# Optimization experiments

Measured on AMD Instinct MI355X. Metric: run time of the kernel, lower is better.

Reference implementation:

```python
import jax, jax.numpy as jnp
import numpy as np

N_NODES = 100000
N_EDGES = 1600000
D_FEAT = 48


def sage_conv(x, src, dst, Wl, Wr, b):
    # mean aggregation of neighbor messages x[src] at dst (PyG source_to_target)
    msg_sum = jax.ops.segment_sum(x[src], dst, num_segments=N_NODES)  # [N, d]
    cnt = jax.ops.segment_sum(jnp.ones((src.shape[0],), x.dtype), dst,
                              num_segments=N_NODES)  # [N]
    mean = msg_sum / jnp.maximum(cnt, 1.0)[:, None]
    # out = lin_l(mean neighbors) + lin_r(self); bias only on lin_l (PyG default)
    return mean @ Wl + b + x @ Wr


def setup_inputs() -> dict:
    key = jax.random.key(0)
    ks = jax.random.split(key, 8)
    x = jax.random.normal(ks[0], (N_NODES, D_FEAT), jnp.float32)
    edge_index = jax.random.randint(ks[1], (2, N_EDGES), 0, N_NODES, jnp.int64)
    def w(k, fi, fo):
        return jax.random.normal(k, (fi, fo), jnp.float32) / np.sqrt(fi)
    return {
        "x": x,
        "edge_index": edge_index,
        "W1l": w(ks[2], D_FEAT, 32), "W1r": w(ks[3], D_FEAT, 32),
        "b1": jnp.zeros((32,), jnp.float32),
        "W2l": w(ks[4], 32, 16), "W2r": w(ks[5], 32, 16),
        "b2": jnp.zeros((16,), jnp.float32),
        "Wlin": w(ks[6], 16, 2), "blin": jnp.zeros((2,), jnp.float32),
    }


def reference(x, edge_index, W1l, W1r, b1, W2l, W2r, b2, Wlin, blin):
    src, dst = edge_index[0], edge_index[1]
    h = jax.nn.relu(sage_conv(x, src, dst, W1l, W1r, b1))
    h = jax.nn.relu(sage_conv(h, src, dst, W2l, W2r, b2))
    return h @ Wlin + blin  # [N, 2] logits
```

## Files before the change

### kernel.cpp

```cpp
#include <hip/hip_runtime.h>
#include <hip/hip_bf16.h>


constexpr int NN  = 100000;
constexpr int NE  = 1600000;
constexpr int NCH = (NN + 255) / 256;
constexpr int NB  = 391;
constexpr int CAP = 4608;
constexpr int SEG = CAP + 3 * 256;
constexpr int T1  = 2048;
constexpr int EPT = T1 / 256;
constexpr int NB1 = (NE + T1 - 1) / T1;

__device__ __forceinline__ float bl(unsigned u) { return __uint_as_float(u << 16); }
__device__ __forceinline__ float bh(unsigned u) { return __uint_as_float(u & 0xffff0000u); }
__device__ __forceinline__ unsigned f2b(float x) {
    unsigned u = __float_as_uint(x);
    return (u + 0x7fffu + ((u >> 16) & 1u)) >> 16;
}
__device__ __forceinline__ unsigned pack2(float a, float b) {
    return f2b(a) | (f2b(b) << 16);
}

__device__ __forceinline__ int wave_incl_scan(int v, int lane) {
#pragma unroll
    for (int d = 1; d < 64; d <<= 1) {
        int t = __shfl_up(v, d, 64);
        if (lane >= d) v += t;
    }
    return v;
}

__global__ __launch_bounds__(256) void k1_kernel(
    const float* __restrict__ X,
    const float* __restrict__ Wl,
    const float* __restrict__ Wr,
    const int*   __restrict__ ei,
    int* __restrict__ bsize, unsigned* __restrict__ bbuf,
    __hip_bfloat16* __restrict__ P, __hip_bfloat16* __restrict__ R)
{
    __shared__ float sW[2][48 * 32];
    __shared__ int hist[NB], base[NB], cur[NB];
    __shared__ int s_any;

    if (blockIdx.x < NCH) {
        for (int i = threadIdx.x; i < 48 * 32; i += 256) {
            sW[0][i] = Wl[i];
            sW[1][i] = Wr[i];
        }
        __syncthreads();
        int n = blockIdx.x * 256 + threadIdx.x;
        if (n > NN) return;
        if (n == NN) {
            uint4 z = make_uint4(0, 0, 0, 0);
            uint4* pp = reinterpret_cast<uint4*>(P + (size_t)NN * 32);
#pragma unroll
            for (int i = 0; i < 4; ++i) pp[i] = z;
            return;
        }
        float xr[48];
        const float4* xp = reinterpret_cast<const float4*>(X + (size_t)n * 48);
#pragma unroll
        for (int i = 0; i < 12; ++i) {
            float4 u = xp[i];
            xr[i*4+0] = u.x; xr[i*4+1] = u.y; xr[i*4+2] = u.z; xr[i*4+3] = u.w;
        }
        float accp[32], accr[32];
#pragma unroll
        for (int j = 0; j < 32; ++j) { accp[j] = 0.f; accr[j] = 0.f; }
#pragma unroll
        for (int k = 0; k < 48; ++k) {
            float xk = xr[k];
#pragma unroll
            for (int j = 0; j < 32; ++j) {
                accp[j] += xk * sW[0][k * 32 + j];
                accr[j] += xk * sW[1][k * 32 + j];
            }
        }
        uint4* pp = reinterpret_cast<uint4*>(P + (size_t)n * 32);
        uint4* rp = reinterpret_cast<uint4*>(R + (size_t)n * 32);
#pragma unroll
        for (int i = 0; i < 4; ++i) {
            uint4 u, v;
            u.x = pack2(accp[i*8+0], accp[i*8+1]); u.y = pack2(accp[i*8+2], accp[i*8+3]);
            u.z = pack2(accp[i*8+4], accp[i*8+5]); u.w = pack2(accp[i*8+6], accp[i*8+7]);
            v.x = pack2(accr[i*8+0], accr[i*8+1]); v.y = pack2(accr[i*8+2], accr[i*8+3]);
            v.z = pack2(accr[i*8+4], accr[i*8+5]); v.w = pack2(accr[i*8+6], accr[i*8+7]);
            pp[i] = u;
            rp[i] = v;
        }
    } else {
        if (threadIdx.x == 0) s_any = 0;
        for (int i = threadIdx.x; i < NB; i += 256) { hist[i] = 0; cur[i] = 0; }
        __syncthreads();
        int dv = 0;
        for (int i = threadIdx.x; i < 2048; i += 256) dv |= ei[2 * i + 1];
        if (dv != 0) atomicOr(&s_any, 1);
        __syncthreads();
        int sh = (s_any == 0) ? 1 : 0;

        int e0 = (blockIdx.x - NCH) * T1;
        int sreg[EPT], dreg[EPT];
#pragma unroll
        for (int it = 0; it < EPT; ++it) {
            int e = e0 + it * 256 + threadIdx.x;
            bool ok = e < NE;
            int s = ok ? ei[(size_t)e << sh] : -1;
            int d = ok ? ei[(size_t)(NE + e) << sh] : -1;
            if ((unsigned)s >= (unsigned)NN || (unsigned)d >= (unsigned)NN) { s = -1; d = -1; }
            sreg[it] = s; dreg[it] = d;
            if (d >= 0) atomicAdd(&hist[d >> 8], 1);
        }
        __syncthreads();
        for (int b = threadIdx.x; b < NB; b += 256) {
            int h = hist[b];
            base[b] = h ? atomicAdd(&bsize[b], h) : 0;
        }
        __syncthreads();
#pragma unroll
        for (int it = 0; it < EPT; ++it) {
            int s = sreg[it], d = dreg[it];
            if (d < 0) continue;
            int b = d >> 8;
            int pos = base[b] + atomicAdd(&cur[b], 1);
            if (pos < CAP)
                bbuf[(size_t)b * CAP + pos] = ((unsigned)s << 8) | (unsigned)(d & 255);
        }
    }
}

__global__ __launch_bounds__(256) void k2_kernel(
    const int* __restrict__ bsize, const unsigned* __restrict__ bbuf,
    int* __restrict__ deg, int* __restrict__ rowstart, int* __restrict__ csr_src)
{
    __shared__ int ldeg[256], lcur[256], ws[4];
    int b = blockIdx.x, t = threadIdx.x;
    int bs = b * SEG;

    int S = min(bsize[b], CAP);
    const unsigned* bp = bbuf + (size_t)b * CAP;
    ldeg[t] = 0;
    __syncthreads();
    for (int i = t; i < S; i += 256)
        atomicAdd(&ldeg[bp[i] & 255u], 1);
    __syncthreads();

    int v  = ldeg[t];
    int pv = (v + 3) & ~3;
    int lane = t & 63, wid = t >> 6;
    int incl = wave_incl_scan(pv, lane);
    if (lane == 63) ws[wid] = incl;
    __syncthreads();
    int off = 0;
#pragma unroll
    for (int w = 0; w < 3; ++w)
        if (wid > w) off += ws[w];
    int excl = off + incl - pv;

    int node = (b << 8) + t;
    if (node < NN) {
        deg[node] = v;
        rowstart[node] = bs + excl;
    }
    lcur[t] = excl;
    __syncthreads();

    for (int i = t; i < S; i += 256) {
        unsigned pk = bp[i];
        int pos = atomicAdd(&lcur[pk & 255u], 1);
        csr_src[bs + pos] = (int)(pk >> 8);
    }
    for (int p = excl + v; p < excl + pv; ++p)
        csr_src[bs + p] = NN;
}

__global__ __launch_bounds__(256) void gather1f_kernel(
    const int* __restrict__ rowstart, const int* __restrict__ deg,
    const int* __restrict__ csr_src,
    const __hip_bfloat16* __restrict__ p1,
    const __hip_bfloat16* __restrict__ r1,
    const float* __restrict__ b1,
    const float* __restrict__ W2l,
    const float* __restrict__ W2r,
    __hip_bfloat16* __restrict__ P2,
    __hip_bfloat16* __restrict__ R2)
{
    __shared__ float sW2l[32 * 16], sW2r[32 * 16], sb1[32];
    __shared__ float shh[32 * 64];
    int t = threadIdx.x;
    for (int i = t; i < 32 * 16; i += 256) { sW2l[i] = W2l[i]; sW2r[i] = W2r[i]; }
    if (t < 32) sb1[t] = b1[t];
    __syncthreads();

    int loc = t >> 2, c = t & 3;
    int n = blockIdx.x * 64 + loc;
    bool valid = n < NN;

    if (valid) {
        int start = rowstart[n], dn = deg[n];
        int pv4 = ((dn + 3) & ~3) >> 2;
        float acc[8];
#pragma unroll
        for (int j = 0; j < 8; ++j) acc[j] = 0.f;
        const uint4* prow = reinterpret_cast<const uint4*>(p1);
        const int4* cp4 = reinterpret_cast<const int4*>(csr_src + start);
        for (int k = 0; k < pv4; ++k) {
            int4 s4 = cp4[k];
            uint4 a = prow[(size_t)s4.x * 4 + c];
            uint4 b = prow[(size_t)s4.y * 4 + c];
            uint4 d = prow[(size_t)s4.z * 4 + c];
            uint4 e = prow[(size_t)s4.w * 4 + c];
            acc[0] += bl(a.x) + bl(b.x) + bl(d.x) + bl(e.x);
            acc[1] += bh(a.x) + bh(b.x) + bh(d.x) + bh(e.x);
            acc[2] += bl(a.y) + bl(b.y) + bl(d.y) + bl(e.y);
            acc[3] += bh(a.y) + bh(b.y) + bh(d.y) + bh(e.y);
            acc[4] += bl(a.z) + bl(b.z) + bl(d.z) + bl(e.z);
            acc[5] += bh(a.z) + bh(b.z) + bh(d.z) + bh(e.z);
            acc[6] += bl(a.w) + bl(b.w) + bl(d.w) + bl(e.w);
            acc[7] += bh(a.w) + bh(b.w) + bh(d.w) + bh(e.w);
        }
        float inv = 1.0f / fmaxf((float)dn, 1.0f);
        uint4 r = reinterpret_cast<const uint4*>(r1)[(size_t)n * 4 + c];
        float rr[8] = { bl(r.x), bh(r.x), bl(r.y), bh(r.y),
                        bl(r.z), bh(r.z), bl(r.w), bh(r.w) };
#pragma unroll
        for (int j = 0; j < 8; ++j)
            shh[(c * 8 + j) * 64 + loc] = fmaxf(acc[j] * inv + rr[j] + sb1[c * 8 + j], 0.f);
    }
    __syncthreads();

    if (valid) {
        float accp[4], accr[4];
#pragma unroll
        for (int j = 0; j < 4; ++j) { accp[j] = 0.f; accr[j] = 0.f; }
#pragma unroll
        for (int k = 0; k < 32; ++k) {
            float hk = shh[k * 64 + loc];
#pragma unroll
            for (int j = 0; j < 4; ++j) {
                accp[j] += hk * sW2l[k * 16 + c * 4 + j];
                accr[j] += hk * sW2r[k * 16 + c * 4 + j];
            }
        }
        uint2 up, ur;
        up.x = pack2(accp[0], accp[1]); up.y = pack2(accp[2], accp[3]);
        ur.x = pack2(accr[0], accr[1]); ur.y = pack2(accr[2], accr[3]);
        reinterpret_cast<uint2*>(P2)[(size_t)n * 4 + c] = up;
        reinterpret_cast<uint2*>(R2)[(size_t)n * 4 + c] = ur;
    } else if (n == NN) {
        uint2 z = make_uint2(0, 0);
        reinterpret_cast<uint2*>(P2)[(size_t)NN * 4 + c] = z;
        reinterpret_cast<uint2*>(R2)[(size_t)NN * 4 + c] = z;
    }
}

__global__ __launch_bounds__(256) void gather2_kernel(
    const int* __restrict__ rowstart, const int* __restrict__ deg,
    const int* __restrict__ csr_src,
    const __hip_bfloat16* __restrict__ P2,
    const __hip_bfloat16* __restrict__ R2,
    const float* __restrict__ b2,
    const float* __restrict__ Wlin,
    const float* __restrict__ blin,
    float* __restrict__ out)
{
    __shared__ float sb[16], sW[32], sbl[2];
    if (threadIdx.x < 16) sb[threadIdx.x] = b2[threadIdx.x];
    else if (threadIdx.x < 48) sW[threadIdx.x - 16] = Wlin[threadIdx.x - 16];
    else if (threadIdx.x < 50) sbl[threadIdx.x - 48] = blin[threadIdx.x - 48];
    __syncthreads();
    int t = blockIdx.x * 256 + threadIdx.x;
    int n = t >> 1, c = t & 1;
    if (n >= NN) return;
    int start = rowstart[n], dn = deg[n];
    int pv4 = ((dn + 3) & ~3) >> 2;

    float acc[8];
#pragma unroll
    for (int j = 0; j < 8; ++j) acc[j] = 0.f;
    const uint4* prow = reinterpret_cast<const uint4*>(P2);
    const int4* cp4 = reinterpret_cast<const int4*>(csr_src + start);
    for (int k = 0; k < pv4; ++k) {
        int4 s4 = cp4[k];
        uint4 a = prow[(size_t)s4.x * 2 + c];
        uint4 b = prow[(size_t)s4.y * 2 + c];
        uint4 d = prow[(size_t)s4.z * 2 + c];
        uint4 e = prow[(size_t)s4.w * 2 + c];
        acc[0] += bl(a.x) + bl(b.x) + bl(d.x) + bl(e.x);
        acc[1] += bh(a.x) + bh(b.x) + bh(d.x) + bh(e.x);
        acc[2] += bl(a.y) + bl(b.y) + bl(d.y) + bl(e.y);
        acc[3] += bh(a.y) + bh(b.y) + bh(d.y) + bh(e.y);
        acc[4] += bl(a.z) + bl(b.z) + bl(d.z) + bl(e.z);
        acc[5] += bh(a.z) + bh(b.z) + bh(d.z) + bh(e.z);
        acc[6] += bl(a.w) + bl(b.w) + bl(d.w) + bl(e.w);
        acc[7] += bh(a.w) + bh(b.w) + bh(d.w) + bh(e.w);
    }
    float inv = 1.0f / fmaxf((float)dn, 1.0f);
    uint4 r = reinterpret_cast<const uint4*>(R2)[(size_t)n * 2 + c];
    float rr[8] = { bl(r.x), bh(r.x), bl(r.y), bh(r.y),
                    bl(r.z), bh(r.z), bl(r.w), bh(r.w) };
    float o0 = 0.f, o1 = 0.f;
#pragma unroll
    for (int j = 0; j < 8; ++j) {
        int kk = c * 8 + j;
        float hv = fmaxf(acc[j] * inv + rr[j] + sb[kk], 0.f);
        o0 += hv * sW[kk * 2];
        o1 += hv * sW[kk * 2 + 1];
    }
    o0 += __shfl_xor(o0, 1, 64);
    o1 += __shfl_xor(o1, 1, 64);
    if (c == 0)
        reinterpret_cast<float2*>(out)[n] = make_float2(o0 + sbl[0], o1 + sbl[1]);
}

extern "C" void kernel_launch(void* const* d_in, const int* in_sizes, int n_in,
                              void* d_out, int out_size, void* d_ws, size_t ws_size,
                              hipStream_t stream)
{
    const float* x    = (const float*)d_in[0];
    const int*   ei   = (const int*)d_in[1];
    const float* W1l  = (const float*)d_in[2];
    const float* W1r  = (const float*)d_in[3];
    const float* b1   = (const float*)d_in[4];
    const float* W2l  = (const float*)d_in[5];
    const float* W2r  = (const float*)d_in[6];
    const float* b2   = (const float*)d_in[7];
    const float* Wlin = (const float*)d_in[8];
    const float* blin = (const float*)d_in[9];
    float* out = (float*)d_out;

    char* wsb = (char*)d_ws;
    int*      bsize    = (int*)(wsb + 64);
    int*      deg      = (int*)(wsb + 4096);
    int*      rowstart = (int*)(wsb + 404096);
    int*      csr_src  = (int*)(wsb + 804096);
    unsigned* bbuf     = (unsigned*)(wsb + 9300000);
    __hip_bfloat16* p1 = (__hip_bfloat16*)(wsb + 16600000);
    __hip_bfloat16* r1 = (__hip_bfloat16*)(wsb + 23100000);
    __hip_bfloat16* p2 = (__hip_bfloat16*)(wsb + 29600000);
    __hip_bfloat16* r2 = (__hip_bfloat16*)(wsb + 32900000);

    dim3 blk(256);

    hipMemsetAsync(bsize, 0, NB * sizeof(int), stream);
    k1_kernel<<<NCH + NB1, blk, 0, stream>>>(x, W1l, W1r, ei, bsize, bbuf, p1, r1);
    k2_kernel<<<NB, blk, 0, stream>>>(bsize, bbuf, deg, rowstart, csr_src);
    gather1f_kernel<<<(NN + 1 + 63) / 64, blk, 0, stream>>>(
        rowstart, deg, csr_src, p1, r1, b1, W2l, W2r, p2, r2);
    gather2_kernel<<<(NN * 2 + 255) / 256, blk, 0, stream>>>(
        rowstart, deg, csr_src, p2, r2, b2, Wlin, blin, out);
}
```

Before: 187.1 us.

## Vectorize edge reads, split dense pass, widen CSR build, prefetch gather indices

```diff
diff --git a/kernel.cpp b/kernel.cpp
--- a/kernel.cpp
+++ b/kernel.cpp
@@ -9,7 +9,6 @@
 constexpr int CAP = 4608;
 constexpr int SEG = CAP + 3 * 256;
 constexpr int T1  = 2048;
-constexpr int EPT = T1 / 256;
 constexpr int NB1 = (NE + T1 - 1) / T1;
 
 __device__ __forceinline__ float bl(unsigned u) { return __uint_as_float(u << 16); }
@@ -31,7 +30,7 @@
     return v;
 }
 
-__global__ __launch_bounds__(256) void k1_kernel(
+__global__ __launch_bounds__(256, 6) void k1_kernel(
     const float* __restrict__ X,
     const float* __restrict__ Wl,
     const float* __restrict__ Wr,
@@ -40,7 +39,7 @@
     __hip_bfloat16* __restrict__ P, __hip_bfloat16* __restrict__ R)
 {
     __shared__ float sW[2][48 * 32];
-    __shared__ int hist[NB], base[NB], cur[NB];
+    __shared__ int hist[NB], base[NB];
     __shared__ int s_any;
 
     if (blockIdx.x < NCH) {
@@ -58,78 +57,108 @@
             for (int i = 0; i < 4; ++i) pp[i] = z;
             return;
         }
-        float xr[48];
         const float4* xp = reinterpret_cast<const float4*>(X + (size_t)n * 48);
-#pragma unroll
-        for (int i = 0; i < 12; ++i) {
-            float4 u = xp[i];
-            xr[i*4+0] = u.x; xr[i*4+1] = u.y; xr[i*4+2] = u.z; xr[i*4+3] = u.w;
-        }
-        float accp[32], accr[32];
-#pragma unroll
-        for (int j = 0; j < 32; ++j) { accp[j] = 0.f; accr[j] = 0.f; }
-#pragma unroll
-        for (int k = 0; k < 48; ++k) {
-            float xk = xr[k];
-#pragma unroll
-            for (int j = 0; j < 32; ++j) {
-                accp[j] += xk * sW[0][k * 32 + j];
-                accr[j] += xk * sW[1][k * 32 + j];
-            }
-        }
-        uint4* pp = reinterpret_cast<uint4*>(P + (size_t)n * 32);
-        uint4* rp = reinterpret_cast<uint4*>(R + (size_t)n * 32);
-#pragma unroll
-        for (int i = 0; i < 4; ++i) {
-            uint4 u, v;
-            u.x = pack2(accp[i*8+0], accp[i*8+1]); u.y = pack2(accp[i*8+2], accp[i*8+3]);
-            u.z = pack2(accp[i*8+4], accp[i*8+5]); u.w = pack2(accp[i*8+6], accp[i*8+7]);
-            v.x = pack2(accr[i*8+0], accr[i*8+1]); v.y = pack2(accr[i*8+2], accr[i*8+3]);
-            v.z = pack2(accr[i*8+4], accr[i*8+5]); v.w = pack2(accr[i*8+6], accr[i*8+7]);
-            pp[i] = u;
-            rp[i] = v;
+        float acc[32];
+#pragma unroll 1
+        for (int pass = 0; pass < 2; ++pass) {
+#pragma unroll
+            for (int j = 0; j < 32; ++j) acc[j] = 0.f;
+#pragma unroll
+            for (int i = 0; i < 12; ++i) {
+                float4 u = xp[i];
+                const float* w = &sW[pass][i * 4 * 32];
+#pragma unroll
+                for (int j = 0; j < 32; ++j) {
+                    acc[j] += u.x * w[j];
+                    acc[j] += u.y * w[32 + j];
+                    acc[j] += u.z * w[64 + j];
+                    acc[j] += u.w * w[96 + j];
+                }
+            }
+            __hip_bfloat16* dstp = pass ? R : P;
+            uint4* op = reinterpret_cast<uint4*>(dstp + (size_t)n * 32);
+#pragma unroll
+            for (int i = 0; i < 4; ++i) {
+                uint4 o;
+                o.x = pack2(acc[i*8+0], acc[i*8+1]);
+                o.y = pack2(acc[i*8+2], acc[i*8+3]);
+                o.z = pack2(acc[i*8+4], acc[i*8+5]);
+                o.w = pack2(acc[i*8+6], acc[i*8+7]);
+                op[i] = o;
+            }
         }
     } else {
         if (threadIdx.x == 0) s_any = 0;
-        for (int i = threadIdx.x; i < NB; i += 256) { hist[i] = 0; cur[i] = 0; }
+        for (int i = threadIdx.x; i < NB; i += 256) hist[i] = 0;
         __syncthreads();
         int dv = 0;
         for (int i = threadIdx.x; i < 2048; i += 256) dv |= ei[2 * i + 1];
         if (dv != 0) atomicOr(&s_any, 1);
         __syncthreads();
-        int sh = (s_any == 0) ? 1 : 0;
-
-        int e0 = (blockIdx.x - NCH) * T1;
-        int sreg[EPT], dreg[EPT];
-#pragma unroll
-        for (int it = 0; it < EPT; ++it) {
-            int e = e0 + it * 256 + threadIdx.x;
-            bool ok = e < NE;
-            int s = ok ? ei[(size_t)e << sh] : -1;
-            int d = ok ? ei[(size_t)(NE + e) << sh] : -1;
-            if ((unsigned)s >= (unsigned)NN || (unsigned)d >= (unsigned)NN) { s = -1; d = -1; }
-            sreg[it] = s; dreg[it] = d;
-            if (d >= 0) atomicAdd(&hist[d >> 8], 1);
-        }
+        const bool i64 = (s_any == 0);
+        const int e0 = (blockIdx.x - NCH) * T1;
+
+        auto sweep = [&](auto&& f) {
+            if (i64) {
+                const int4* sp = reinterpret_cast<const int4*>(ei) + (e0 >> 1);
+                const int4* dp = reinterpret_cast<const int4*>(ei) + ((NE + e0) >> 1);
+#pragma unroll
+                for (int it = 0; it < 4; ++it) {
+                    int p = it * 256 + threadIdx.x;
+                    int e = e0 + 2 * p;
+                    if (e + 2 <= NE) {
+                        int4 s4 = sp[p], d4 = dp[p];
+                        f(s4.x, d4.x);
+                        f(s4.z, d4.z);
+                    } else {
+                        for (int e2 = e; e2 < NE && e2 < e + 2; ++e2)
+                            f(ei[(size_t)e2 << 1], ei[(size_t)(NE + e2) << 1]);
+                    }
+                }
+            } else {
+                const int4* sp = reinterpret_cast<const int4*>(ei) + (e0 >> 2);
+                const int4* dp = reinterpret_cast<const int4*>(ei) + ((NE + e0) >> 2);
+#pragma unroll
+                for (int it = 0; it < 2; ++it) {
+                    int q = it * 256 + threadIdx.x;
+                    int e = e0 + 4 * q;
+                    if (e + 4 <= NE) {
+                        int4 s4 = sp[q], d4 = dp[q];
+                        f(s4.x, d4.x);
+                        f(s4.y, d4.y);
+                        f(s4.z, d4.z);
+                        f(s4.w, d4.w);
+                    } else {
+                        for (int e2 = e; e2 < NE && e2 < e + 4; ++e2)
+                            f(ei[e2], ei[NE + e2]);
+                    }
+                }
+            }
+        };
+
+        sweep([&](int s, int d) {
+            if ((unsigned)s < (unsigned)NN && (unsigned)d < (unsigned)NN)
+                atomicAdd(&hist[d >> 8], 1);
+        });
         __syncthreads();
         for (int b = threadIdx.x; b < NB; b += 256) {
             int h = hist[b];
             base[b] = h ? atomicAdd(&bsize[b], h) : 0;
         }
         __syncthreads();
-#pragma unroll
-        for (int it = 0; it < EPT; ++it) {
-            int s = sreg[it], d = dreg[it];
-            if (d < 0) continue;
-            int b = d >> 8;
-            int pos = base[b] + atomicAdd(&cur[b], 1);
-            if (pos < CAP)
-                bbuf[(size_t)b * CAP + pos] = ((unsigned)s << 8) | (unsigned)(d & 255);
-        }
-    }
-}
-
-__global__ __launch_bounds__(256) void k2_kernel(
+        sweep([&](int s, int d) {
+            if ((unsigned)s < (unsigned)NN && (unsigned)d < (unsigned)NN) {
+                int bk = d >> 8;
+                int pos = atomicAdd(&base[bk], 1);
+                if (pos < CAP)
+                    bbuf[(size_t)bk * CAP + pos] =
+                        ((unsigned)s << 8) | (unsigned)(d & 255);
+            }
+        });
+    }
+}
+
+__global__ __launch_bounds__(1024) void k2_kernel(
     const int* __restrict__ bsize, const unsigned* __restrict__ bbuf,
     int* __restrict__ deg, int* __restrict__ rowstart, int* __restrict__ csr_src)
 {
@@ -139,39 +168,43 @@
 
     int S = min(bsize[b], CAP);
     const unsigned* bp = bbuf + (size_t)b * CAP;
-    ldeg[t] = 0;
-    __syncthreads();
-    for (int i = t; i < S; i += 256)
+    if (t < 256) ldeg[t] = 0;
+    __syncthreads();
+    for (int i = t; i < S; i += 1024)
         atomicAdd(&ldeg[bp[i] & 255u], 1);
     __syncthreads();
 
-    int v  = ldeg[t];
-    int pv = (v + 3) & ~3;
-    int lane = t & 63, wid = t >> 6;
-    int incl = wave_incl_scan(pv, lane);
-    if (lane == 63) ws[wid] = incl;
-    __syncthreads();
-    int off = 0;
-#pragma unroll
-    for (int w = 0; w < 3; ++w)
-        if (wid > w) off += ws[w];
-    int excl = off + incl - pv;
-
-    int node = (b << 8) + t;
-    if (node < NN) {
-        deg[node] = v;
-        rowstart[node] = bs + excl;
-    }
-    lcur[t] = excl;
-    __syncthreads();
-
-    for (int i = t; i < S; i += 256) {
+    int v = 0, pv = 0, incl = 0, excl = 0;
+    if (t < 256) {
+        v  = ldeg[t];
+        pv = (v + 3) & ~3;
+        incl = wave_incl_scan(pv, t & 63);
+        if ((t & 63) == 63) ws[t >> 6] = incl;
+    }
+    __syncthreads();
+    if (t < 256) {
+        int off = 0, wid = t >> 6;
+#pragma unroll
+        for (int w = 0; w < 3; ++w)
+            if (wid > w) off += ws[w];
+        excl = off + incl - pv;
+        int node = (b << 8) + t;
+        if (node < NN) {
+            deg[node] = v;
+            rowstart[node] = bs + excl;
+        }
+        lcur[t] = excl;
+    }
+    __syncthreads();
+
+    for (int i = t; i < S; i += 1024) {
         unsigned pk = bp[i];
         int pos = atomicAdd(&lcur[pk & 255u], 1);
         csr_src[bs + pos] = (int)(pk >> 8);
     }
-    for (int p = excl + v; p < excl + pv; ++p)
-        csr_src[bs + p] = NN;
+    if (t < 256)
+        for (int p = excl + v; p < excl + pv; ++p)
+            csr_src[bs + p] = NN;
 }
 
 __global__ __launch_bounds__(256) void gather1f_kernel(
@@ -186,7 +219,7 @@
     __hip_bfloat16* __restrict__ R2)
 {
     __shared__ float sW2l[32 * 16], sW2r[32 * 16], sb1[32];
-    __shared__ float shh[32 * 64];
+    __shared__ float shh[32 * 65];
     int t = threadIdx.x;
     for (int i = t; i < 32 * 16; i += 256) { sW2l[i] = W2l[i]; sW2r[i] = W2r[i]; }
     if (t < 32) sb1[t] = b1[t];
@@ -199,13 +232,15 @@
     if (valid) {
         int start = rowstart[n], dn = deg[n];
         int pv4 = ((dn + 3) & ~3) >> 2;
-        float acc[8];
-#pragma unroll
-        for (int j = 0; j < 8; ++j) acc[j] = 0.f;
         const uint4* prow = reinterpret_cast<const uint4*>(p1);
         const int4* cp4 = reinterpret_cast<const int4*>(csr_src + start);
+        uint4 r = reinterpret_cast<const uint4*>(r1)[(size_t)n * 4 + c];
+        float acc[8];
+#pragma unroll
+        for (int j = 0; j < 8; ++j) acc[j] = 0.f;
+        int4 s4 = cp4[0];
         for (int k = 0; k < pv4; ++k) {
-            int4 s4 = cp4[k];
+            int4 nx = cp4[k + 1];
             uint4 a = prow[(size_t)s4.x * 4 + c];
             uint4 b = prow[(size_t)s4.y * 4 + c];
             uint4 d = prow[(size_t)s4.z * 4 + c];
@@ -218,14 +253,14 @@
             acc[5] += bh(a.z) + bh(b.z) + bh(d.z) + bh(e.z);
             acc[6] += bl(a.w) + bl(b.w) + bl(d.w) + bl(e.w);
             acc[7] += bh(a.w) + bh(b.w) + bh(d.w) + bh(e.w);
+            s4 = nx;
         }
         float inv = 1.0f / fmaxf((float)dn, 1.0f);
-        uint4 r = reinterpret_cast<const uint4*>(r1)[(size_t)n * 4 + c];
         float rr[8] = { bl(r.x), bh(r.x), bl(r.y), bh(r.y),
                         bl(r.z), bh(r.z), bl(r.w), bh(r.w) };
 #pragma unroll
         for (int j = 0; j < 8; ++j)
-            shh[(c * 8 + j) * 64 + loc] = fmaxf(acc[j] * inv + rr[j] + sb1[c * 8 + j], 0.f);
+            shh[(c * 8 + j) * 65 + loc] = fmaxf(acc[j] * inv + rr[j] + sb1[c * 8 + j], 0.f);
     }
     __syncthreads();
 
@@ -235,7 +270,7 @@
         for (int j = 0; j < 4; ++j) { accp[j] = 0.f; accr[j] = 0.f; }
 #pragma unroll
         for (int k = 0; k < 32; ++k) {
-            float hk = shh[k * 64 + loc];
+            float hk = shh[k * 65 + loc];
 #pragma unroll
             for (int j = 0; j < 4; ++j) {
                 accp[j] += hk * sW2l[k * 16 + c * 4 + j];
@@ -275,13 +310,15 @@
     int start = rowstart[n], dn = deg[n];
     int pv4 = ((dn + 3) & ~3) >> 2;
 
-    float acc[8];
-#pragma unroll
-    for (int j = 0; j < 8; ++j) acc[j] = 0.f;
     const uint4* prow = reinterpret_cast<const uint4*>(P2);
     const int4* cp4 = reinterpret_cast<const int4*>(csr_src + start);
+    uint4 r = reinterpret_cast<const uint4*>(R2)[(size_t)n * 2 + c];
+    float acc[8];
+#pragma unroll
+    for (int j = 0; j < 8; ++j) acc[j] = 0.f;
+    int4 s4 = cp4[0];
     for (int k = 0; k < pv4; ++k) {
-        int4 s4 = cp4[k];
+        int4 nx = cp4[k + 1];
         uint4 a = prow[(size_t)s4.x * 2 + c];
         uint4 b = prow[(size_t)s4.y * 2 + c];
         uint4 d = prow[(size_t)s4.z * 2 + c];
@@ -294,9 +331,9 @@
         acc[5] += bh(a.z) + bh(b.z) + bh(d.z) + bh(e.z);
         acc[6] += bl(a.w) + bl(b.w) + bl(d.w) + bl(e.w);
         acc[7] += bh(a.w) + bh(b.w) + bh(d.w) + bh(e.w);
+        s4 = nx;
     }
     float inv = 1.0f / fmaxf((float)dn, 1.0f);
-    uint4 r = reinterpret_cast<const uint4*>(R2)[(size_t)n * 2 + c];
     float rr[8] = { bl(r.x), bh(r.x), bl(r.y), bh(r.y),
                     bl(r.z), bh(r.z), bl(r.w), bh(r.w) };
     float o0 = 0.f, o1 = 0.f;
@@ -344,7 +381,7 @@
 
     hipMemsetAsync(bsize, 0, NB * sizeof(int), stream);
     k1_kernel<<<NCH + NB1, blk, 0, stream>>>(x, W1l, W1r, ei, bsize, bbuf, p1, r1);
-    k2_kernel<<<NB, blk, 0, stream>>>(bsize, bbuf, deg, rowstart, csr_src);
+    k2_kernel<<<NB, dim3(1024), 0, stream>>>(bsize, bbuf, deg, rowstart, csr_src);
     gather1f_kernel<<<(NN + 1 + 63) / 64, blk, 0, stream>>>(
         rowstart, deg, csr_src, p1, r1, b1, W2l, W2r, p2, r2);
     gather2_kernel<<<(NN * 2 + 255) / 256, blk, 0, stream>>>(
```

Result: slower. 498.9 us (+166.7%).
